# Kernel optimization log

Hardware: AMD Instinct MI355X
Metric: run time of the kernel (lower is better)

Reference implementation:

```python
import jax, jax.numpy as jnp
import numpy as np

S, B, H, D, IN = 512, 8, 8, 64, 512  # seq, batch, heads, head dim, model dim
PROJ = H * (5 * D + 2)


def setup_inputs() -> dict:
    key = jax.random.key(0)
    k0, k1, k2 = jax.random.split(key, 3)
    x = jax.random.normal(k0, (S, B, IN), jnp.float32)
    W_slow = jax.random.normal(k1, (PROJ, IN), jnp.float32) / np.sqrt(IN).astype(np.float32)
    W_out = jax.random.normal(k2, (IN, H * D), jnp.float32) / np.sqrt(H * D).astype(np.float32)
    ln_gamma = jnp.ones((IN,), jnp.float32)
    ln_beta = jnp.zeros((IN,), jnp.float32)
    return dict(x=x, W_slow=W_slow, W_out=W_out, ln_gamma=ln_gamma, ln_beta=ln_beta)


def reference(x, W_slow, W_out, ln_gamma, ln_beta):
    slen, bsz, in_dim = x.shape
    # pre-LayerNorm (torch LayerNorm: biased variance, eps=1e-5)
    mu = x.mean(-1, keepdims=True)
    var = x.var(-1, keepdims=True)
    normed = (x - mu) / jnp.sqrt(var + 1e-5) * ln_gamma + ln_beta
    qkvb = (normed @ W_slow.T).reshape(slen, bsz, H, 5 * D + 2)
    q, k, v, rk, rv, beta, rbeta = jnp.split(
        qkvb, [D, 2 * D, 3 * D, 4 * D, 5 * D, 5 * D + 1], axis=-1)
    q = jax.nn.softmax(q, axis=-1)
    k = jax.nn.softmax(k, axis=-1)
    rk = jax.nn.softmax(rk, axis=-1)
    beta = jax.nn.sigmoid(beta)    # (S,B,H,1)
    rbeta = jax.nn.sigmoid(rbeta)  # (S,B,H,1)

    # ---- fast_weight_memory: delta-rule fast weight, z_t = W_t q_t ----
    W0 = jnp.zeros((bsz, H, D, D), x.dtype)

    def fw_step(W, inp):
        qt, kt, vt, bt = inp  # (B,H,D),(B,H,D),(B,H,D),(B,H,1)
        v_old = jnp.einsum('bhij,bhj->bhi', W, kt)
        W = W + (bt * (vt - v_old))[..., :, None] * kt[..., None, :]
        z = jnp.einsum('bhij,bhj->bhi', W, qt)
        return W, z

    _, z = jax.lax.scan(fw_step, W0, (q, k, v, beta))  # z: (S,B,H,D)

    # ---- fast_rnn_v2: recurrent fast weight, h_t = z_t + R_t softmax(h_{t-1}) ----
    R0 = jnp.zeros((bsz, H, D, D), x.dtype)
    h0 = jnp.zeros((bsz, H, D), x.dtype)

    def rec_step(carry, inp):
        R, h = carry
        zt, kt, vt, bt = inp
        qh = jax.nn.softmax(h, axis=-1)
        v_old = jnp.einsum('bhij,bhj->bhi', R, kt)
        R = R + (bt * (vt - v_old))[..., :, None] * kt[..., None, :]
        h = zt + jnp.einsum('bhij,bhj->bhi', R, qh)
        return (R, h), h

    _, hs = jax.lax.scan(rec_step, (R0, h0), (z, rk, rv, rbeta))  # (S,B,H,D)

    out = hs.reshape(slen, bsz, H * D) @ W_out.T  # (S,B,IN)
    # dropout = 0.0 -> identity; residual
    return x + out
```

## Files before the change

kernel.cpp:

```cpp
#include <hip/hip_runtime.h>

#define S_LEN 512
#define BSZ 8
#define NH 8
#define HD 64
#define IN_DIM 512
#define PROJ 2576
#define SEG 322
#define AST 352
#define CHUNK 8
#define NCH 64
#define CB (CHUNK * AST * 4)

typedef __attribute__((ext_vector_type(8))) __bf16 bf16x8;
typedef __attribute__((ext_vector_type(4))) float f32x4;

static __device__ __forceinline__ unsigned short f2bf(float f) {
  unsigned u = __float_as_uint(f);
  unsigned r = (u + 0x7fffu + ((u >> 16) & 1u)) >> 16;
  return (unsigned short)r;
}
static __device__ __forceinline__ float bf2f(unsigned short s) {
  return __uint_as_float(((unsigned)s) << 16);
}

static __device__ __forceinline__ void gl_lds16(const void* g, void* l) {
  __builtin_amdgcn_global_load_lds(
      (const __attribute__((address_space(1))) unsigned int*)g,
      (__attribute__((address_space(3))) unsigned int*)l, 16, 0, 0);
}

__global__ __launch_bounds__(256) void ln_kernel(const float* __restrict__ x,
                                                 const float* __restrict__ gamma,
                                                 const float* __restrict__ beta,
                                                 unsigned short* __restrict__ out) {
  int wave = threadIdx.x >> 6, lane = threadIdx.x & 63;
  int row = blockIdx.x * 4 + wave;
  const float* xr = x + (size_t)row * IN_DIM + lane * 8;
  float4 a = *(const float4*)xr;
  float4 b = *(const float4*)(xr + 4);
  float vals[8] = {a.x, a.y, a.z, a.w, b.x, b.y, b.z, b.w};
  float s = 0.f, ss = 0.f;
#pragma unroll
  for (int i = 0; i < 8; i++) { s += vals[i]; ss += vals[i] * vals[i]; }
#pragma unroll
  for (int o = 32; o; o >>= 1) { s += __shfl_xor(s, o); ss += __shfl_xor(ss, o); }
  float mu = s * (1.f / 512.f);
  float var = ss * (1.f / 512.f) - mu * mu;
  float rstd = rsqrtf(var + 1e-5f);
  const float* g = gamma + lane * 8;
  const float* be = beta + lane * 8;
  float4 g1 = *(const float4*)g, g2 = *(const float4*)(g + 4);
  float4 b1 = *(const float4*)be, b2 = *(const float4*)(be + 4);
  float gs[8] = {g1.x, g1.y, g1.z, g1.w, g2.x, g2.y, g2.z, g2.w};
  float bs[8] = {b1.x, b1.y, b1.z, b1.w, b2.x, b2.y, b2.z, b2.w};
  union { unsigned short u[8]; uint4 v; } pk;
#pragma unroll
  for (int i = 0; i < 8; i++) pk.u[i] = f2bf((vals[i] - mu) * rstd * gs[i] + bs[i]);
  *(uint4*)(out + (size_t)row * IN_DIM + lane * 8) = pk.v;
}

__global__ void cast_kernel(const float* __restrict__ in, unsigned short* __restrict__ out, int n) {
  int i = blockIdx.x * blockDim.x + threadIdx.x;
  int st = gridDim.x * blockDim.x;
  for (; i < n; i += st) out[i] = f2bf(in[i]);
}

template <int BF16_OUT, int RESID>
__global__ __launch_bounds__(256) void gemm_bt(const unsigned short* __restrict__ A,
                                               const unsigned short* __restrict__ B,
                                               void* __restrict__ Cout,
                                               const float* __restrict__ resid,
                                               int M, int N, int K) {
  __shared__ __align__(16) unsigned short As[64][40];
  __shared__ __align__(16) unsigned short Bs[64][40];
  int tid = threadIdx.x;
  int lane = tid & 63, wave = tid >> 6;
  int m0 = blockIdx.y * 64, n0 = blockIdx.x * 64;
  int srow = tid >> 2, skq = (tid & 3) * 8;
  const unsigned short* Ap = A + (size_t)(m0 + srow) * K + skq;
  const unsigned short* Bp = B + (size_t)(n0 + srow) * K + skq;
  bool bvalid = (n0 + srow) < N;
  f32x4 zero = {0.f, 0.f, 0.f, 0.f};
  f32x4 acc[4];
#pragma unroll
  for (int nt = 0; nt < 4; nt++) acc[nt] = zero;
  int q = lane >> 4, m16 = lane & 15;
  for (int k0 = 0; k0 < K; k0 += 32) {
    uint4 av = *(const uint4*)(Ap + k0);
    uint4 bz = {0u, 0u, 0u, 0u};
    uint4 bv = bvalid ? *(const uint4*)(Bp + k0) : bz;
    *(uint4*)&As[srow][skq] = av;
    *(uint4*)&Bs[srow][skq] = bv;
    __syncthreads();
    bf16x8 af = *(const bf16x8*)&As[wave * 16 + m16][q * 8];
#pragma unroll
    for (int nt = 0; nt < 4; nt++) {
      bf16x8 bfv = *(const bf16x8*)&Bs[nt * 16 + m16][q * 8];
      acc[nt] = __builtin_amdgcn_mfma_f32_16x16x32_bf16(af, bfv, acc[nt], 0, 0, 0);
    }
    __syncthreads();
  }
  int rbase = q * 4;
#pragma unroll
  for (int nt = 0; nt < 4; nt++) {
#pragma unroll
    for (int rr = 0; rr < 4; rr++) {
      int gm = m0 + wave * 16 + rbase + rr;
      int gn = n0 + nt * 16 + m16;
      if (gn < N) {
        float v = acc[nt][rr];
        if (BF16_OUT) {
          ((unsigned short*)Cout)[(size_t)gm * N + gn] = f2bf(v);
        } else {
          float o = v;
          if (RESID) o += resid[(size_t)gm * N + gn];
          ((float*)Cout)[(size_t)gm * N + gn] = o;
        }
      }
    }
  }
}

__global__ __launch_bounds__(256) void act_kernel(const unsigned short* __restrict__ qkvb,
                                                  float* __restrict__ act) {
  int gw = blockIdx.x * 4 + (threadIdx.x >> 6);
  int l = threadIdx.x & 63;
  int m = gw >> 3, hh = gw & 7;
  int t = m >> 3, b = m & 7;
  const unsigned short* src = qkvb + (size_t)m * PROJ + hh * SEG;
  float fq = bf2f(src[l]);
  float fk = bf2f(src[64 + l]);
  float fv = bf2f(src[128 + l]);
  float fr = bf2f(src[192 + l]);
  float frv = bf2f(src[256 + l]);
  float mq = fq, mk = fk, mr = fr;
#pragma unroll
  for (int o = 32; o; o >>= 1) {
    mq = fmaxf(mq, __shfl_xor(mq, o));
    mk = fmaxf(mk, __shfl_xor(mk, o));
    mr = fmaxf(mr, __shfl_xor(mr, o));
  }
  float eq = __expf(fq - mq), ek = __expf(fk - mk), er = __expf(fr - mr);
  float sq = eq, sk = ek, sr = er;
#pragma unroll
  for (int o = 32; o; o >>= 1) {
    sq += __shfl_xor(sq, o);
    sk += __shfl_xor(sk, o);
    sr += __shfl_xor(sr, o);
  }
  int bh = b * 8 + hh;
  float* dst = act + ((size_t)bh * S_LEN + t) * AST;
  dst[l] = eq * __builtin_amdgcn_rcpf(sq);
  dst[64 + l] = ek * __builtin_amdgcn_rcpf(sk);
  dst[128 + l] = er * __builtin_amdgcn_rcpf(sr);
  dst[192 + l] = fv;
  dst[256 + l] = frv;
  if (l < 2) {
    float xv = bf2f(src[320 + l]);
    dst[320 + l] = __builtin_amdgcn_rcpf(1.f + __expf(-xv));
  }
}

__global__ __launch_bounds__(128, 1) void scan_kernel(const float* __restrict__ act,
                                                      unsigned short* __restrict__ hs) {
  int bh = blockIdx.x;
  int b = bh >> 3, hh = bh & 7;
  int tid = threadIdx.x, l = tid & 63, w = tid >> 6;

  __shared__ __align__(16) float stage[4][CHUNK * AST];
  __shared__ __align__(16) float zring[4][CHUNK][64];
  __shared__ __align__(16) float ehb[64];
  __shared__ int flags[16];

  volatile int* w0done = &flags[0];
  volatile int* w1done = &flags[8];

  const char* abase = (const char*)(act + (size_t)bh * S_LEN * AST);

  if (tid == 0) { flags[0] = 0; flags[8] = 0; }
  if (w) ehb[l] = 1.f;
  if (w == 0) {
#pragma unroll
    for (int i = 0; i < 11; i++)
      gl_lds16(abase + (size_t)i * 1024 + l * 16, (char*)&stage[0][0] + i * 1024);
  }
  __syncthreads();

  f32x4 M[16];
#pragma unroll
  for (int j = 0; j < 16; j++) M[j] = (f32x4){0.f, 0.f, 0.f, 0.f};
  const f32x4 z4 = {0.f, 0.f, 0.f, 0.f};

  if (w == 0) {
    for (int c = 0; c < NCH; c++) {
      if (c >= 3) {
        while (*w1done < c - 2) __builtin_amdgcn_s_sleep(2);
      }
      if (c + 1 < NCH) {
        const char* nb = abase + (size_t)(c + 1) * CB;
        char* sb = (char*)&stage[(c + 1) & 3][0];
#pragma unroll
        for (int i = 0; i < 11; i++)
          gl_lds16(nb + (size_t)i * 1024 + l * 16, sb + i * 1024);
        asm volatile("s_waitcnt vmcnt(11)" ::: "memory");
      } else {
        asm volatile("s_waitcnt vmcnt(0)" ::: "memory");
      }
      const float* cb = &stage[c & 3][0];
      float* zc = &zring[c & 3][0][0];
#pragma unroll
      for (int s = 0; s < CHUNK; s++) {
        const float* stf = cb + s * AST;
        const f32x4* st4 = (const f32x4*)stf;
        float cv = stf[192 + l];
        f32x4 kk[16];
#pragma unroll
        for (int j = 0; j < 16; j++) kk[j] = st4[16 + j];
        f32x4 a0 = z4, a1 = z4, a2 = z4, a3 = z4;
#pragma unroll
        for (int j = 0; j < 16; j += 4) {
          a0 += M[j] * kk[j];
          a1 += M[j + 1] * kk[j + 1];
          a2 += M[j + 2] * kk[j + 2];
          a3 += M[j + 3] * kk[j + 3];
        }
        f32x4 vo = (a0 + a1) + (a2 + a3);
        float vold = (vo.x + vo.y) + (vo.z + vo.w);
        float bt = stf[320];
        float coef = bt * (cv - vold);
        f32x4 c4 = {coef, coef, coef, coef};
        a0 = a1 = a2 = a3 = z4;
#pragma unroll
        for (int j = 0; j < 16; j += 4) {
          M[j] += c4 * kk[j];         a0 += M[j] * st4[j];
          M[j + 1] += c4 * kk[j + 1]; a1 += M[j + 1] * st4[j + 1];
          M[j + 2] += c4 * kk[j + 2]; a2 += M[j + 2] * st4[j + 2];
          M[j + 3] += c4 * kk[j + 3]; a3 += M[j + 3] * st4[j + 3];
        }
        vo = (a0 + a1) + (a2 + a3);
        zc[s * 64 + l] = (vo.x + vo.y) + (vo.z + vo.w);
      }
      asm volatile("s_waitcnt lgkmcnt(0)" ::: "memory");
      *w0done = c + 1;
    }
  } else {
    unsigned short* hdst = hs + (size_t)b * 512 + hh * 64 + l;
    for (int c = 0; c < NCH; c++) {
      while (*w0done < c + 1) __builtin_amdgcn_s_sleep(2);
      const float* cb = &stage[c & 3][0];
      const float* zc = &zring[c & 3][0][0];
#pragma unroll
      for (int s = 0; s < CHUNK; s++) {
        const float* stf = cb + s * AST;
        const f32x4* st4 = (const f32x4*)stf;
        float z = zc[s * 64 + l];
        float cv = stf[256 + l];
        f32x4 kk[16];
#pragma unroll
        for (int j = 0; j < 16; j++) kk[j] = st4[32 + j];
        f32x4 a0 = z4, a1 = z4, a2 = z4, a3 = z4;
#pragma unroll
        for (int j = 0; j < 16; j += 4) {
          a0 += M[j] * kk[j];
          a1 += M[j + 1] * kk[j + 1];
          a2 += M[j + 2] * kk[j + 2];
          a3 += M[j + 3] * kk[j + 3];
        }
        f32x4 vo = (a0 + a1) + (a2 + a3);
        float rvold = (vo.x + vo.y) + (vo.z + vo.w);
        float rb = stf[321];
        float rcoef = rb * (cv - rvold);
        f32x4 c4 = {rcoef, rcoef, rcoef, rcoef};
        const f32x4* e4 = (const f32x4*)ehb;
        f32x4 s0 = z4, s1 = z4, s2v = z4, s3 = z4;
        a0 = a1 = a2 = a3 = z4;
#pragma unroll
        for (int j = 0; j < 16; j += 4) {
          f32x4 e0 = e4[j], e1 = e4[j + 1], e2 = e4[j + 2], e3 = e4[j + 3];
          M[j] += c4 * kk[j];         a0 += M[j] * e0;       s0 += e0;
          M[j + 1] += c4 * kk[j + 1]; a1 += M[j + 1] * e1;   s1 += e1;
          M[j + 2] += c4 * kk[j + 2]; a2 += M[j + 2] * e2;   s2v += e2;
          M[j + 3] += c4 * kk[j + 3]; a3 += M[j + 3] * e3;   s3 += e3;
        }
        f32x4 ho = (a0 + a1) + (a2 + a3);
        f32x4 so = (s0 + s1) + (s2v + s3);
        float hp = (ho.x + ho.y) + (ho.z + ho.w);
        float sm = (so.x + so.y) + (so.z + so.w);
        float h = z + hp * __builtin_amdgcn_rcpf(sm);
        hdst[(size_t)(c * CHUNK + s) * (BSZ * 512)] = f2bf(h);
        ehb[l] = __expf(h - 20.f);
      }
      asm volatile("s_waitcnt lgkmcnt(0)" ::: "memory");
      *w1done = c + 1;
    }
  }
}

extern "C" void kernel_launch(void* const* d_in, const int* in_sizes, int n_in,
                              void* d_out, int out_size, void* d_ws, size_t ws_size,
                              hipStream_t stream) {
  const float* x = (const float*)d_in[0];
  const float* W_slow = (const float*)d_in[1];
  const float* W_out = (const float*)d_in[2];
  const float* gamma = (const float*)d_in[3];
  const float* beta = (const float*)d_in[4];

  char* ws = (char*)d_ws;
  size_t off = 0;
  unsigned short* normed = (unsigned short*)(ws + off); off += (size_t)4096 * 512 * 2;
  unsigned short* Wslow_b = (unsigned short*)(ws + off); off += (size_t)PROJ * 512 * 2;
  unsigned short* Wout_b = (unsigned short*)(ws + off); off += (size_t)512 * 512 * 2;
  unsigned short* qkvb = (unsigned short*)(ws + off); off += (size_t)4096 * PROJ * 2;
  float* act = (float*)(ws + off); off += (size_t)64 * S_LEN * AST * 4;
  unsigned short* hsb = normed;

  hipLaunchKernelGGL(ln_kernel, dim3(1024), dim3(256), 0, stream, x, gamma, beta, normed);
  hipLaunchKernelGGL(cast_kernel, dim3(512), dim3(256), 0, stream, W_slow, Wslow_b, PROJ * 512);
  hipLaunchKernelGGL(cast_kernel, dim3(256), dim3(256), 0, stream, W_out, Wout_b, 512 * 512);
  hipLaunchKernelGGL((gemm_bt<1, 0>), dim3((PROJ + 63) / 64, 4096 / 64), dim3(256), 0, stream,
                     normed, Wslow_b, (void*)qkvb, (const float*)nullptr, 4096, PROJ, 512);
  hipLaunchKernelGGL(act_kernel, dim3(8192), dim3(256), 0, stream, qkvb, act);
  hipLaunchKernelGGL(scan_kernel, dim3(64), dim3(128), 0, stream, act, hsb);
  hipLaunchKernelGGL((gemm_bt<0, 1>), dim3(512 / 64, 4096 / 64), dim3(256), 0, stream,
                     hsb, Wout_b, d_out, x, 4096, 512, 512);
}
```

Baseline: 404.3 us.

## Take rank-1 update off the critical path via algebraic z/h reformulation

In both recurrent scans, the output W_t q_t is rewritten as W_{t-1} q_t + coef*(k_t·q_t). This lets the old-state products with k and q (or with softmax(h)) run in one fused pass, with the scalar dot computed by a wave shuffle reduction. The rank-1 state update moves after the output is produced, so it no longer sits between the two matvecs on the serial dependency chain. The softmax denominator is also computed once per step by a shuffle reduction rather than re-summed inside the loop. The cost is extra cross-lane shuffles and slightly different float rounding order.

```diff
diff --git a/kernel.cpp b/kernel.cpp
--- a/kernel.cpp
+++ b/kernel.cpp
@@ -213,39 +213,42 @@
       for (int s = 0; s < CHUNK; s++) {
         const float* stf = cb + s * AST;
         const f32x4* st4 = (const f32x4*)stf;
+        float kl = stf[64 + l], ql = stf[l];
         float cv = stf[192 + l];
-        f32x4 kk[16];
-#pragma unroll
-        for (int j = 0; j < 16; j++) kk[j] = st4[16 + j];
+        float bt = stf[320];
+        float kq = kl * ql;
+#pragma unroll
+        for (int o = 32; o; o >>= 1) kq += __shfl_xor(kq, o);
         f32x4 a0 = z4, a1 = z4, a2 = z4, a3 = z4;
+        f32x4 b0 = z4, b1 = z4, b2 = z4, b3 = z4;
 #pragma unroll
         for (int j = 0; j < 16; j += 4) {
-          a0 += M[j] * kk[j];
-          a1 += M[j + 1] * kk[j + 1];
-          a2 += M[j + 2] * kk[j + 2];
-          a3 += M[j + 3] * kk[j + 3];
+          f32x4 k0 = st4[16 + j], q0 = st4[j];
+          a0 += M[j] * k0;      b0 += M[j] * q0;
+          f32x4 k1 = st4[17 + j], q1 = st4[j + 1];
+          a1 += M[j + 1] * k1;  b1 += M[j + 1] * q1;
+          f32x4 k2 = st4[18 + j], q2 = st4[j + 2];
+          a2 += M[j + 2] * k2;  b2 += M[j + 2] * q2;
+          f32x4 k3 = st4[19 + j], q3 = st4[j + 3];
+          a3 += M[j + 3] * k3;  b3 += M[j + 3] * q3;
         }
         f32x4 vo = (a0 + a1) + (a2 + a3);
+        f32x4 bo = (b0 + b1) + (b2 + b3);
         float vold = (vo.x + vo.y) + (vo.z + vo.w);
-        float bt = stf[320];
         float coef = bt * (cv - vold);
+        float zq = (bo.x + bo.y) + (bo.z + bo.w);
+        zc[s * 64 + l] = zq + coef * kq;
         f32x4 c4 = {coef, coef, coef, coef};
-        a0 = a1 = a2 = a3 = z4;
-#pragma unroll
-        for (int j = 0; j < 16; j += 4) {
-          M[j] += c4 * kk[j];         a0 += M[j] * st4[j];
-          M[j + 1] += c4 * kk[j + 1]; a1 += M[j + 1] * st4[j + 1];
-          M[j + 2] += c4 * kk[j + 2]; a2 += M[j + 2] * st4[j + 2];
-          M[j + 3] += c4 * kk[j + 3]; a3 += M[j + 3] * st4[j + 3];
-        }
-        vo = (a0 + a1) + (a2 + a3);
-        zc[s * 64 + l] = (vo.x + vo.y) + (vo.z + vo.w);
+#pragma unroll
+        for (int j = 0; j < 16; j++) M[j] += c4 * st4[16 + j];
       }
       asm volatile("s_waitcnt lgkmcnt(0)" ::: "memory");
       *w0done = c + 1;
     }
   } else {
     unsigned short* hdst = hs + (size_t)b * 512 + hh * 64 + l;
+    float ehl = 1.f;
+    float smn = 64.f;
     for (int c = 0; c < NCH; c++) {
       while (*w0done < c + 1) __builtin_amdgcn_s_sleep(2);
       const float* cb = &stage[c & 3][0];
@@ -254,42 +257,48 @@
       for (int s = 0; s < CHUNK; s++) {
         const float* stf = cb + s * AST;
         const f32x4* st4 = (const f32x4*)stf;
-        float z = zc[s * 64 + l];
+        float zv = zc[s * 64 + l];
+        float rkl = stf[128 + l];
         float cv = stf[256 + l];
-        f32x4 kk[16];
-#pragma unroll
-        for (int j = 0; j < 16; j++) kk[j] = st4[32 + j];
+        float rb = stf[321];
+        float pr = rkl * ehl;
+#pragma unroll
+        for (int o = 32; o; o >>= 1) pr += __shfl_xor(pr, o);
+        const f32x4* e4 = (const f32x4*)ehb;
         f32x4 a0 = z4, a1 = z4, a2 = z4, a3 = z4;
+        f32x4 b0 = z4, b1 = z4, b2 = z4, b3 = z4;
 #pragma unroll
         for (int j = 0; j < 16; j += 4) {
-          a0 += M[j] * kk[j];
-          a1 += M[j + 1] * kk[j + 1];
-          a2 += M[j + 2] * kk[j + 2];
-          a3 += M[j + 3] * kk[j + 3];
+          f32x4 k0 = st4[32 + j];
+          a0 += M[j] * k0;
+          f32x4 k1 = st4[33 + j];
+          a1 += M[j + 1] * k1;
+          f32x4 k2 = st4[34 + j];
+          a2 += M[j + 2] * k2;
+          f32x4 k3 = st4[35 + j];
+          a3 += M[j + 3] * k3;
+          f32x4 e0 = e4[j], e1 = e4[j + 1], e2 = e4[j + 2], e3 = e4[j + 3];
+          b0 += M[j] * e0;
+          b1 += M[j + 1] * e1;
+          b2 += M[j + 2] * e2;
+          b3 += M[j + 3] * e3;
         }
         f32x4 vo = (a0 + a1) + (a2 + a3);
+        f32x4 bo = (b0 + b1) + (b2 + b3);
         float rvold = (vo.x + vo.y) + (vo.z + vo.w);
-        float rb = stf[321];
         float rcoef = rb * (cv - rvold);
+        float hpe = (bo.x + bo.y) + (bo.z + bo.w);
+        float hp = hpe + rcoef * pr;
+        float h = zv + hp * __builtin_amdgcn_rcpf(smn);
+        hdst[(size_t)(c * CHUNK + s) * (BSZ * 512)] = f2bf(h);
+        ehl = __expf(h - 20.f);
+        ehb[l] = ehl;
+        smn = ehl;
+#pragma unroll
+        for (int o = 32; o; o >>= 1) smn += __shfl_xor(smn, o);
         f32x4 c4 = {rcoef, rcoef, rcoef, rcoef};
-        const f32x4* e4 = (const f32x4*)ehb;
-        f32x4 s0 = z4, s1 = z4, s2v = z4, s3 = z4;
-        a0 = a1 = a2 = a3 = z4;
-#pragma unroll
-        for (int j = 0; j < 16; j += 4) {
-          f32x4 e0 = e4[j], e1 = e4[j + 1], e2 = e4[j + 2], e3 = e4[j + 3];
-          M[j] += c4 * kk[j];         a0 += M[j] * e0;       s0 += e0;
-          M[j + 1] += c4 * kk[j + 1]; a1 += M[j + 1] * e1;   s1 += e1;
-          M[j + 2] += c4 * kk[j + 2]; a2 += M[j + 2] * e2;   s2v += e2;
-          M[j + 3] += c4 * kk[j + 3]; a3 += M[j + 3] * e3;   s3 += e3;
-        }
-        f32x4 ho = (a0 + a1) + (a2 + a3);
-        f32x4 so = (s0 + s1) + (s2v + s3);
-        float hp = (ho.x + ho.y) + (ho.z + ho.w);
-        float sm = (so.x + so.y) + (so.z + so.w);
-        float h = z + hp * __builtin_amdgcn_rcpf(sm);
-        hdst[(size_t)(c * CHUNK + s) * (BSZ * 512)] = f2bf(h);
-        ehb[l] = __expf(h - 20.f);
+#pragma unroll
+        for (int j = 0; j < 16; j++) M[j] += c4 * st4[32 + j];
       }
       asm volatile("s_waitcnt lgkmcnt(0)" ::: "memory");
       *w1done = c + 1;
```

New measurement: 589.9 us. 45.9% more time.

## Use 128x128 tiled MFMA GEMM with direct global-to-LDS loads

Applied to the files above, without the earlier changes.

Replaces the 64x64 bf16 GEMM with a 128x128 block tile in which each wave computes a 64x64 sub-tile using a 4x4 grid of MFMA accumulators. Operands are loaded straight from global memory into LDS through a gl_lds16 helper, and out-of-range B rows are clamped instead of zero-filled. The aim is to cut global and LDS traffic per FLOP and raise MFMA density in both projection GEMMs. In exchange the grids get smaller (only 128 blocks for the output GEMM), register pressure rises, and there is still no double buffering.

```diff
diff --git a/kernel.cpp b/kernel.cpp
--- a/kernel.cpp
+++ b/kernel.cpp
@@ -67,55 +67,78 @@
 }
 
 template <int BF16_OUT, int RESID>
-__global__ __launch_bounds__(256) void gemm_bt(const unsigned short* __restrict__ A,
+__global__ __launch_bounds__(256) void gemm128(const unsigned short* __restrict__ A,
                                                const unsigned short* __restrict__ B,
                                                void* __restrict__ Cout,
                                                const float* __restrict__ resid,
                                                int M, int N, int K) {
-  __shared__ __align__(16) unsigned short As[64][40];
-  __shared__ __align__(16) unsigned short Bs[64][40];
+  __shared__ __align__(16) unsigned short As[128 * 32];
+  __shared__ __align__(16) unsigned short Bs[128 * 32];
   int tid = threadIdx.x;
-  int lane = tid & 63, wave = tid >> 6;
-  int m0 = blockIdx.y * 64, n0 = blockIdx.x * 64;
-  int srow = tid >> 2, skq = (tid & 3) * 8;
-  const unsigned short* Ap = A + (size_t)(m0 + srow) * K + skq;
-  const unsigned short* Bp = B + (size_t)(n0 + srow) * K + skq;
-  bool bvalid = (n0 + srow) < N;
-  f32x4 zero = {0.f, 0.f, 0.f, 0.f};
-  f32x4 acc[4];
-#pragma unroll
-  for (int nt = 0; nt < 4; nt++) acc[nt] = zero;
+  int lane = tid & 63, w = tid >> 6;
+  int wr = w >> 1, wc = w & 1;
+  int m0 = blockIdx.y * 128, n0 = blockIdx.x * 128;
+
+  int r0 = (w * 2) * 16 + (lane >> 2);
+  int r1 = (w * 2 + 1) * 16 + (lane >> 2);
+  int kq = (lane & 3) * 8;
+  const unsigned short* A0 = A + (size_t)(m0 + r0) * K + kq;
+  const unsigned short* A1 = A + (size_t)(m0 + r1) * K + kq;
+  int bn0 = n0 + r0; if (bn0 > N - 1) bn0 = N - 1;
+  int bn1 = n0 + r1; if (bn1 > N - 1) bn1 = N - 1;
+  const unsigned short* B0 = B + (size_t)bn0 * K + kq;
+  const unsigned short* B1 = B + (size_t)bn1 * K + kq;
+  char* asb0 = (char*)As + (w * 2) * 1024;
+  char* asb1 = (char*)As + (w * 2 + 1) * 1024;
+  char* bsb0 = (char*)Bs + (w * 2) * 1024;
+  char* bsb1 = (char*)Bs + (w * 2 + 1) * 1024;
+
+  f32x4 acc[4][4];
+#pragma unroll
+  for (int i = 0; i < 4; i++)
+#pragma unroll
+    for (int j = 0; j < 4; j++) acc[i][j] = (f32x4){0.f, 0.f, 0.f, 0.f};
+
   int q = lane >> 4, m16 = lane & 15;
   for (int k0 = 0; k0 < K; k0 += 32) {
-    uint4 av = *(const uint4*)(Ap + k0);
-    uint4 bz = {0u, 0u, 0u, 0u};
-    uint4 bv = bvalid ? *(const uint4*)(Bp + k0) : bz;
-    *(uint4*)&As[srow][skq] = av;
-    *(uint4*)&Bs[srow][skq] = bv;
+    gl_lds16(A0 + k0, asb0);
+    gl_lds16(A1 + k0, asb1);
+    gl_lds16(B0 + k0, bsb0);
+    gl_lds16(B1 + k0, bsb1);
+    asm volatile("s_waitcnt vmcnt(0)" ::: "memory");
     __syncthreads();
-    bf16x8 af = *(const bf16x8*)&As[wave * 16 + m16][q * 8];
-#pragma unroll
-    for (int nt = 0; nt < 4; nt++) {
-      bf16x8 bfv = *(const bf16x8*)&Bs[nt * 16 + m16][q * 8];
-      acc[nt] = __builtin_amdgcn_mfma_f32_16x16x32_bf16(af, bfv, acc[nt], 0, 0, 0);
-    }
+    bf16x8 af[4], bfv[4];
+#pragma unroll
+    for (int f = 0; f < 4; f++)
+      af[f] = *(const bf16x8*)&As[(wr * 64 + f * 16 + m16) * 32 + q * 8];
+#pragma unroll
+    for (int f = 0; f < 4; f++)
+      bfv[f] = *(const bf16x8*)&Bs[(wc * 64 + f * 16 + m16) * 32 + q * 8];
+#pragma unroll
+    for (int fa = 0; fa < 4; fa++)
+#pragma unroll
+      for (int fb = 0; fb < 4; fb++)
+        acc[fa][fb] = __builtin_amdgcn_mfma_f32_16x16x32_bf16(af[fa], bfv[fb], acc[fa][fb], 0, 0, 0);
     __syncthreads();
   }
-  int rbase = q * 4;
-#pragma unroll
-  for (int nt = 0; nt < 4; nt++) {
-#pragma unroll
-    for (int rr = 0; rr < 4; rr++) {
-      int gm = m0 + wave * 16 + rbase + rr;
-      int gn = n0 + nt * 16 + m16;
-      if (gn < N) {
-        float v = acc[nt][rr];
-        if (BF16_OUT) {
-          ((unsigned short*)Cout)[(size_t)gm * N + gn] = f2bf(v);
-        } else {
-          float o = v;
-          if (RESID) o += resid[(size_t)gm * N + gn];
-          ((float*)Cout)[(size_t)gm * N + gn] = o;
+
+#pragma unroll
+  for (int fa = 0; fa < 4; fa++) {
+#pragma unroll
+    for (int fb = 0; fb < 4; fb++) {
+#pragma unroll
+      for (int rr = 0; rr < 4; rr++) {
+        int gm = m0 + wr * 64 + fa * 16 + q * 4 + rr;
+        int gn = n0 + wc * 64 + fb * 16 + m16;
+        if (gn < N) {
+          float v = acc[fa][fb][rr];
+          if (BF16_OUT) {
+            ((unsigned short*)Cout)[(size_t)gm * N + gn] = f2bf(v);
+          } else {
+            float o = v;
+            if (RESID) o += resid[(size_t)gm * N + gn];
+            ((float*)Cout)[(size_t)gm * N + gn] = o;
+          }
         }
       }
     }
@@ -318,10 +341,10 @@
   hipLaunchKernelGGL(ln_kernel, dim3(1024), dim3(256), 0, stream, x, gamma, beta, normed);
   hipLaunchKernelGGL(cast_kernel, dim3(512), dim3(256), 0, stream, W_slow, Wslow_b, PROJ * 512);
   hipLaunchKernelGGL(cast_kernel, dim3(256), dim3(256), 0, stream, W_out, Wout_b, 512 * 512);
-  hipLaunchKernelGGL((gemm_bt<1, 0>), dim3((PROJ + 63) / 64, 4096 / 64), dim3(256), 0, stream,
+  hipLaunchKernelGGL((gemm128<1, 0>), dim3((PROJ + 127) / 128, 4096 / 128), dim3(256), 0, stream,
                      normed, Wslow_b, (void*)qkvb, (const float*)nullptr, 4096, PROJ, 512);
   hipLaunchKernelGGL(act_kernel, dim3(8192), dim3(256), 0, stream, qkvb, act);
   hipLaunchKernelGGL(scan_kernel, dim3(64), dim3(128), 0, stream, act, hsb);
-  hipLaunchKernelGGL((gemm_bt<0, 1>), dim3(512 / 64, 4096 / 64), dim3(256), 0, stream,
+  hipLaunchKernelGGL((gemm128<0, 1>), dim3(512 / 128, 4096 / 128), dim3(256), 0, stream,
                      hsb, Wout_b, d_out, x, 4096, 512, 512);
 }
```

Result: no change. 402.2 us (-0.5%).
